# Performance work log

Hardware: AMD Instinct MI355X
Metric: run time of the kernel (lower is better)

## Reference

```python
import jax, jax.numpy as jnp
import numpy as np

# AccumulateKnn with distances == 1.0 everywhere and n_moments=0:
# weight w = exp(-distance) = exp(-1); output = concat(mean_k(w*f), max_k(w*f))
_W = float(np.exp(-1.0))


def _accumulate_knn(features, idx):
    # features: [N, F], idx: [N, K] -> [N, 2F]
    g = features[idx]                      # [N, K, F] neighbour gather
    mean = jnp.mean(g, axis=1) * _W        # [N, F]
    mx = jnp.max(g, axis=1) * _W           # [N, F]
    return jnp.concatenate([mean, mx], axis=-1)


def setup_inputs() -> dict:
    key = jax.random.key(0)
    k1, k2, k3, k4 = jax.random.split(key, 4)
    N, K, F = 200000, 32, 64
    x = jax.random.normal(k1, (N, F), dtype=jnp.float32)
    neighbour_indices = jax.random.randint(k2, (N, K), 0, N, dtype=jnp.int64)
    W0 = jax.random.normal(k3, (F, 64), dtype=jnp.float32) * (1.0 / np.sqrt(F))
    b0 = jnp.zeros((64,), dtype=jnp.float32)
    W1 = jax.random.normal(k4, (128, 64), dtype=jnp.float32) * (1.0 / np.sqrt(128))
    b1 = jnp.zeros((64,), dtype=jnp.float32)
    return {"x": x, "neighbour_indices": neighbour_indices,
            "W0": W0, "b0": b0, "W1": W1, "b1": b1}


def reference(x, neighbour_indices, W0, b0, W1, b1):
    allfeat = []
    feats = x
    for (W, b) in ((W0, b0), (W1, b1)):
        f = jax.nn.relu(feats @ W + b)            # dense + ReLU, [N, F_i]
        coll = _accumulate_knn(f, neighbour_indices)  # [N, 2*F_i]
        # subtract tiled self features: tile(f,[1,2]) == concat([f,f],-1)
        out = coll - jnp.concatenate([f, f], axis=-1)
        allfeat.append(out)
        feats = out
    return jnp.concatenate(allfeat + [x], axis=-1)  # [N, 128+128+64]
```

## Files before the change

kernel.cpp:

```cpp
#include <hip/hip_runtime.h>
#include <hip/hip_bf16.h>

typedef __hip_bfloat16 bf16;
typedef __attribute__((ext_vector_type(8))) short short8;
typedef __attribute__((ext_vector_type(4))) float f32x4;

__device__ __forceinline__ float us2f(unsigned short u) {
  union { unsigned int ui; float f; } cv; cv.ui = ((unsigned int)u) << 16; return cv.f;
}
__device__ __forceinline__ unsigned short f2us(float f) {
  union { float f; unsigned int u; } cv; cv.f = f;
  unsigned int u = cv.u;
  return (unsigned short)((u + 0x7fffu + ((u >> 16) & 1u)) >> 16);
}
__device__ __forceinline__ float lo2f(unsigned int u) {
  union { unsigned int ui; float f; } cv; cv.ui = u << 16; return cv.f;
}
__device__ __forceinline__ float hi2f(unsigned int u) {
  union { unsigned int ui; float f; } cv; cv.ui = u & 0xffff0000u; return cv.f;
}

#define WEXP 0.36787944117144233f

template<int KDIM>
__global__ __launch_bounds__(256) void dense_mfma_kernel(
    const float* __restrict__ in, int in_stride,
    const float* __restrict__ W, const float* __restrict__ b,
    bf16* __restrict__ fout, float* __restrict__ xcopy, int n)
{
  constexpr int NKS = KDIM / 32;
  constexpr int NFRAG = NKS * 4 * 64;
  __shared__ unsigned short WTf[NFRAG * 8];

  const int tx = threadIdx.x;
#pragma unroll
  for (int fch = 0; fch < NFRAG / 256; ++fch) {
    const int fi = fch * 256 + tx;
    const int ln = fi & 63;
    const int ct = (fi >> 6) & 3;
    const int ks = fi >> 8;
    const int c  = ct * 16 + (ln & 15);
    const int kb = ks * 32 + (ln >> 4) * 8;
    short8 wf;
#pragma unroll
    for (int j = 0; j < 8; ++j)
      wf[j] = (short)f2us(W[(size_t)(kb + j) * 64 + c]);
    *(short8*)&WTf[(size_t)fi * 8] = wf;
  }
  __syncthreads();

  const int wv = tx >> 6;
  const int lane = tx & 63;
  const int mrow = lane & 15;
  const int kgrp = lane >> 4;
  const int row = blockIdx.x * 64 + wv * 16 + mrow;

  f32x4 acc[4] = {};

#pragma unroll
  for (int ks = 0; ks < NKS; ++ks) {
    const int k0 = ks * 32 + kgrp * 8;
    float4 a0 = make_float4(0.f, 0.f, 0.f, 0.f);
    float4 a1 = make_float4(0.f, 0.f, 0.f, 0.f);
    if (row < n) {
      a0 = *(const float4*)(in + (size_t)row * in_stride + k0);
      a1 = *(const float4*)(in + (size_t)row * in_stride + k0 + 4);
    }
    if (xcopy != nullptr && row < n) {
      *(float4*)(xcopy + (size_t)row * 320 + k0) = a0;
      *(float4*)(xcopy + (size_t)row * 320 + k0 + 4) = a1;
    }
    short8 xhi, xlo;
    const float av[8] = {a0.x, a0.y, a0.z, a0.w, a1.x, a1.y, a1.z, a1.w};
#pragma unroll
    for (int j = 0; j < 8; ++j) {
      const unsigned short h = f2us(av[j]);
      xhi[j] = (short)h;
      xlo[j] = (short)f2us(av[j] - us2f(h));
    }
#pragma unroll
    for (int ct = 0; ct < 4; ++ct) {
      const short8 wfr = *(const short8*)&WTf[(size_t)((ks * 4 + ct) * 64 + lane) * 8];
      acc[ct] = __builtin_amdgcn_mfma_f32_16x16x32_bf16(wfr, xhi, acc[ct], 0, 0, 0);
      acc[ct] = __builtin_amdgcn_mfma_f32_16x16x32_bf16(wfr, xlo, acc[ct], 0, 0, 0);
    }
  }

  if (row < n) {
    unsigned short* fr = (unsigned short*)fout + (size_t)row * 64;
#pragma unroll
    for (int ct = 0; ct < 4; ++ct) {
      const int c0 = ct * 16 + kgrp * 4;
      const float4 bb = *(const float4*)&b[c0];
      ushort4 o;
      o.x = f2us(fmaxf(acc[ct][0] + bb.x, 0.f));
      o.y = f2us(fmaxf(acc[ct][1] + bb.y, 0.f));
      o.z = f2us(fmaxf(acc[ct][2] + bb.z, 0.f));
      o.w = f2us(fmaxf(acc[ct][3] + bb.w, 0.f));
      *(ushort4*)&fr[c0] = o;
    }
  }
}

__global__ __launch_bounds__(256) void accum_kernel(
    const bf16* __restrict__ f,
    const int* __restrict__ idx,
    float* __restrict__ out,
    int n)
{
  const int wid = threadIdx.x >> 6;
  const int lane = threadIdx.x & 63;
  const int i = blockIdx.x * 4 + wid;
  if (i >= n) return;

  int iv = 0;
  if (lane < 32) iv = idx[(size_t)i * 32 + lane];

  const int L = lane & 7;
  const int srcbase = (lane >> 3) << 2;
  const char* fb = (const char*)f;

  const uint4 sd = *(const uint4*)(fb + (((unsigned)i) << 7) + ((unsigned)L << 4));

  int nk[4];
#pragma unroll
  for (int t = 0; t < 4; ++t) nk[t] = __shfl(iv, srcbase + t);

  uint4 d[4];
#pragma unroll
  for (int t = 0; t < 4; ++t)
    d[t] = *(const uint4*)(fb + (((unsigned)nk[t]) << 7) + ((unsigned)L << 4));

  float s[8], m[8];
#pragma unroll
  for (int j = 0; j < 8; ++j) { s[j] = 0.f; m[j] = -3.4e38f; }
#pragma unroll
  for (int t = 0; t < 4; ++t) {
    float v;
    v = lo2f(d[t].x); s[0] += v; m[0] = fmaxf(m[0], v);
    v = hi2f(d[t].x); s[1] += v; m[1] = fmaxf(m[1], v);
    v = lo2f(d[t].y); s[2] += v; m[2] = fmaxf(m[2], v);
    v = hi2f(d[t].y); s[3] += v; m[3] = fmaxf(m[3], v);
    v = lo2f(d[t].z); s[4] += v; m[4] = fmaxf(m[4], v);
    v = hi2f(d[t].z); s[5] += v; m[5] = fmaxf(m[5], v);
    v = lo2f(d[t].w); s[6] += v; m[6] = fmaxf(m[6], v);
    v = hi2f(d[t].w); s[7] += v; m[7] = fmaxf(m[7], v);
  }

#pragma unroll
  for (int off = 8; off <= 32; off <<= 1) {
#pragma unroll
    for (int j = 0; j < 8; ++j) {
      s[j] += __shfl_xor(s[j], off);
      m[j] = fmaxf(m[j], __shfl_xor(m[j], off));
    }
  }

  float self[8];
  self[0] = lo2f(sd.x); self[1] = hi2f(sd.x);
  self[2] = lo2f(sd.y); self[3] = hi2f(sd.y);
  self[4] = lo2f(sd.z); self[5] = hi2f(sd.z);
  self[6] = lo2f(sd.w); self[7] = hi2f(sd.w);

  const float cmean = WEXP / 32.0f;
  const int o = lane >> 3;
  float* orow = out + (size_t)i * 320;
  if (o == 0) {
    float4 a, bq;
    a.x = s[0] * cmean - self[0]; a.y = s[1] * cmean - self[1];
    a.z = s[2] * cmean - self[2]; a.w = s[3] * cmean - self[3];
    bq.x = s[4] * cmean - self[4]; bq.y = s[5] * cmean - self[5];
    bq.z = s[6] * cmean - self[6]; bq.w = s[7] * cmean - self[7];
    *(float4*)(orow + 8 * L) = a;
    *(float4*)(orow + 8 * L + 4) = bq;
  } else if (o == 1) {
    float4 a, bq;
    a.x = m[0] * WEXP - self[0]; a.y = m[1] * WEXP - self[1];
    a.z = m[2] * WEXP - self[2]; a.w = m[3] * WEXP - self[3];
    bq.x = m[4] * WEXP - self[4]; bq.y = m[5] * WEXP - self[5];
    bq.z = m[6] * WEXP - self[6]; bq.w = m[7] * WEXP - self[7];
    *(float4*)(orow + 64 + 8 * L) = a;
    *(float4*)(orow + 64 + 8 * L + 4) = bq;
  }
}

extern "C" void kernel_launch(void* const* d_in, const int* in_sizes, int n_in,
                              void* d_out, int out_size, void* d_ws, size_t ws_size,
                              hipStream_t stream) {
  const float* x  = (const float*)d_in[0];
  const int* idx  = (const int*)d_in[1];
  const float* W0 = (const float*)d_in[2];
  const float* b0 = (const float*)d_in[3];
  const float* W1 = (const float*)d_in[4];
  const float* b1 = (const float*)d_in[5];
  float* out = (float*)d_out;
  const int n = in_sizes[0] / 64;

  bf16* fbuf = (bf16*)d_ws;

  const int dblocks = (n + 63) / 64;
  const int ablocks = (n + 3) / 4;

  dense_mfma_kernel<64><<<dblocks, 256, 0, stream>>>(x, 64, W0, b0, fbuf, out + 256, n);
  accum_kernel<<<ablocks, 256, 0, stream>>>(fbuf, idx, out, n);
  dense_mfma_kernel<128><<<dblocks, 256, 0, stream>>>(out, 320, W1, b1, fbuf, nullptr, n);
  accum_kernel<<<ablocks, 256, 0, stream>>>(fbuf, idx, out + 128, n);
}
```

Before: 558.5 us.

## Fuse first kNN accumulation with second dense layer via shared memory

Merges the first accumulate kernel and the second dense MFMA kernel into one kernel. Each 64-row block gathers neighbours, writes the layer-1 output to global memory and also to shared memory, then runs the dense matmul from LDS, so the 128-wide activations are not re-read from global. Gathers are software-pipelined across two register sets, and a second workspace buffer holds the layer-2 features. The fused kernel uses much more shared memory per block (about 50 KB), which may lower occupancy for the latency-bound gather.

```diff
diff --git a/kernel.cpp b/kernel.cpp
--- a/kernel.cpp
+++ b/kernel.cpp
@@ -88,6 +88,204 @@
 
   if (row < n) {
     unsigned short* fr = (unsigned short*)fout + (size_t)row * 64;
+#pragma unroll
+    for (int ct = 0; ct < 4; ++ct) {
+      const int c0 = ct * 16 + kgrp * 4;
+      const float4 bb = *(const float4*)&b[c0];
+      ushort4 o;
+      o.x = f2us(fmaxf(acc[ct][0] + bb.x, 0.f));
+      o.y = f2us(fmaxf(acc[ct][1] + bb.y, 0.f));
+      o.z = f2us(fmaxf(acc[ct][2] + bb.z, 0.f));
+      o.w = f2us(fmaxf(acc[ct][3] + bb.w, 0.f));
+      *(ushort4*)&fr[c0] = o;
+    }
+  }
+}
+
+__global__ __launch_bounds__(256) void accum_dense_fused_kernel(
+    const bf16* __restrict__ f0,
+    const int* __restrict__ idx,
+    const float* __restrict__ W,
+    const float* __restrict__ b,
+    float* __restrict__ out,
+    bf16* __restrict__ f1,
+    int n)
+{
+  __shared__ unsigned short WTf[1024 * 8];
+  __shared__ float SX[64][132];
+
+  const int tx = threadIdx.x;
+  const int p0 = blockIdx.x * 64;
+
+#pragma unroll
+  for (int fch = 0; fch < 4; ++fch) {
+    const int fi = fch * 256 + tx;
+    const int ln = fi & 63;
+    const int ct = (fi >> 6) & 3;
+    const int ks = fi >> 8;
+    const int c  = ct * 16 + (ln & 15);
+    const int kb = ks * 32 + (ln >> 4) * 8;
+    short8 wf;
+#pragma unroll
+    for (int j = 0; j < 8; ++j)
+      wf[j] = (short)f2us(W[(size_t)(kb + j) * 64 + c]);
+    *(short8*)&WTf[(size_t)fi * 8] = wf;
+  }
+
+  const int wv = tx >> 6;
+  const int lane = tx & 63;
+  const int oct = lane >> 3;
+  const unsigned Lo16 = ((unsigned)(lane & 7)) << 4;
+  const char* fb = (const char*)f0;
+  const float cmean = WEXP / 32.0f;
+
+  const uint4* idxv = (const uint4*)(idx + (size_t)(p0 + wv * 16) * 32);
+  uint4 q0 = make_uint4(0u, 0u, 0u, 0u), q1 = make_uint4(0u, 0u, 0u, 0u);
+  if (p0 + wv * 16 + (lane >> 3) < n)     q0 = idxv[lane];
+  if (p0 + wv * 16 + 8 + (lane >> 3) < n) q1 = idxv[64 + lane];
+
+#define ISSUE(pt, SD, D0, D1, D2, D3)                                        \
+  {                                                                          \
+    const uint4 q = ((pt) < 8) ? q0 : q1;                                    \
+    const int srcl = (((pt) & 7) << 3) + oct;                                \
+    const int n0 = __shfl((int)q.x, srcl);                                   \
+    const int n1 = __shfl((int)q.y, srcl);                                   \
+    const int n2 = __shfl((int)q.z, srcl);                                   \
+    const int n3 = __shfl((int)q.w, srcl);                                   \
+    const int ii = p0 + wv * 16 + (pt);                                      \
+    if (ii < n) {                                                            \
+      SD = *(const uint4*)(fb + (((unsigned)ii) << 7) + Lo16);               \
+      D0 = *(const uint4*)(fb + (((unsigned)n0) << 7) + Lo16);               \
+      D1 = *(const uint4*)(fb + (((unsigned)n1) << 7) + Lo16);               \
+      D2 = *(const uint4*)(fb + (((unsigned)n2) << 7) + Lo16);               \
+      D3 = *(const uint4*)(fb + (((unsigned)n3) << 7) + Lo16);               \
+    }                                                                        \
+  }
+
+#define UNP(D)                                                               \
+  { float v;                                                                 \
+    v = lo2f(D.x); s0 += v; m0 = fmaxf(m0, v);                               \
+    v = hi2f(D.x); s1 += v; m1 = fmaxf(m1, v);                               \
+    v = lo2f(D.y); s2 += v; m2 = fmaxf(m2, v);                               \
+    v = hi2f(D.y); s3 += v; m3 = fmaxf(m3, v);                               \
+    v = lo2f(D.z); s4 += v; m4 = fmaxf(m4, v);                               \
+    v = hi2f(D.z); s5 += v; m5 = fmaxf(m5, v);                               \
+    v = lo2f(D.w); s6 += v; m6 = fmaxf(m6, v);                               \
+    v = hi2f(D.w); s7 += v; m7 = fmaxf(m7, v); }
+
+#define BFLY(off)                                                            \
+  { s0 += __shfl_xor(s0, off); m0 = fmaxf(m0, __shfl_xor(m0, off));          \
+    s1 += __shfl_xor(s1, off); m1 = fmaxf(m1, __shfl_xor(m1, off));          \
+    s2 += __shfl_xor(s2, off); m2 = fmaxf(m2, __shfl_xor(m2, off));          \
+    s3 += __shfl_xor(s3, off); m3 = fmaxf(m3, __shfl_xor(m3, off));          \
+    s4 += __shfl_xor(s4, off); m4 = fmaxf(m4, __shfl_xor(m4, off));          \
+    s5 += __shfl_xor(s5, off); m5 = fmaxf(m5, __shfl_xor(m5, off));          \
+    s6 += __shfl_xor(s6, off); m6 = fmaxf(m6, __shfl_xor(m6, off));          \
+    s7 += __shfl_xor(s7, off); m7 = fmaxf(m7, __shfl_xor(m7, off)); }
+
+#define REDUCE(pt, SD, D0, D1, D2, D3)                                       \
+  {                                                                          \
+    float s0 = 0.f, s1 = 0.f, s2 = 0.f, s3 = 0.f,                            \
+          s4 = 0.f, s5 = 0.f, s6 = 0.f, s7 = 0.f;                            \
+    float m0 = -3.4e38f, m1 = -3.4e38f, m2 = -3.4e38f, m3 = -3.4e38f,        \
+          m4 = -3.4e38f, m5 = -3.4e38f, m6 = -3.4e38f, m7 = -3.4e38f;        \
+    UNP(D0) UNP(D1) UNP(D2) UNP(D3)                                          \
+    BFLY(8) BFLY(16) BFLY(32)                                                \
+    const int ii = p0 + wv * 16 + (pt);                                      \
+    if (ii < n) {                                                            \
+      float4 a, bq;                                                          \
+      if (oct == 0) {                                                        \
+        a.x  = s0 * cmean - lo2f(SD.x); a.y  = s1 * cmean - hi2f(SD.x);      \
+        a.z  = s2 * cmean - lo2f(SD.y); a.w  = s3 * cmean - hi2f(SD.y);      \
+        bq.x = s4 * cmean - lo2f(SD.z); bq.y = s5 * cmean - hi2f(SD.z);      \
+        bq.z = s6 * cmean - lo2f(SD.w); bq.w = s7 * cmean - hi2f(SD.w);      \
+        float* orow = out + (size_t)ii * 320 + 8 * (lane & 7);               \
+        *(float4*)orow = a; *(float4*)(orow + 4) = bq;                       \
+        float* sx = &SX[wv * 16 + (pt)][8 * (lane & 7)];                     \
+        *(float4*)sx = a; *(float4*)(sx + 4) = bq;                           \
+      } else if (oct == 1) {                                                 \
+        a.x  = m0 * WEXP - lo2f(SD.x); a.y  = m1 * WEXP - hi2f(SD.x);        \
+        a.z  = m2 * WEXP - lo2f(SD.y); a.w  = m3 * WEXP - hi2f(SD.y);        \
+        bq.x = m4 * WEXP - lo2f(SD.z); bq.y = m5 * WEXP - hi2f(SD.z);        \
+        bq.z = m6 * WEXP - lo2f(SD.w); bq.w = m7 * WEXP - hi2f(SD.w);        \
+        float* orow = out + (size_t)ii * 320 + 64 + 8 * (lane & 7);          \
+        *(float4*)orow = a; *(float4*)(orow + 4) = bq;                       \
+        float* sx = &SX[wv * 16 + (pt)][64 + 8 * (lane & 7)];                \
+        *(float4*)sx = a; *(float4*)(sx + 4) = bq;                           \
+      }                                                                      \
+    }                                                                        \
+  }
+
+  {
+    uint4 sA, a0, a1, a2, a3, sB, b0q, b1q, b2q, b3q;
+    ISSUE(0, sA, a0, a1, a2, a3)
+    ISSUE(1, sB, b0q, b1q, b2q, b3q)
+    REDUCE(0, sA, a0, a1, a2, a3)
+    ISSUE(2, sA, a0, a1, a2, a3)
+    REDUCE(1, sB, b0q, b1q, b2q, b3q)
+    ISSUE(3, sB, b0q, b1q, b2q, b3q)
+    REDUCE(2, sA, a0, a1, a2, a3)
+    ISSUE(4, sA, a0, a1, a2, a3)
+    REDUCE(3, sB, b0q, b1q, b2q, b3q)
+    ISSUE(5, sB, b0q, b1q, b2q, b3q)
+    REDUCE(4, sA, a0, a1, a2, a3)
+    ISSUE(6, sA, a0, a1, a2, a3)
+    REDUCE(5, sB, b0q, b1q, b2q, b3q)
+    ISSUE(7, sB, b0q, b1q, b2q, b3q)
+    REDUCE(6, sA, a0, a1, a2, a3)
+    ISSUE(8, sA, a0, a1, a2, a3)
+    REDUCE(7, sB, b0q, b1q, b2q, b3q)
+    ISSUE(9, sB, b0q, b1q, b2q, b3q)
+    REDUCE(8, sA, a0, a1, a2, a3)
+    ISSUE(10, sA, a0, a1, a2, a3)
+    REDUCE(9, sB, b0q, b1q, b2q, b3q)
+    ISSUE(11, sB, b0q, b1q, b2q, b3q)
+    REDUCE(10, sA, a0, a1, a2, a3)
+    ISSUE(12, sA, a0, a1, a2, a3)
+    REDUCE(11, sB, b0q, b1q, b2q, b3q)
+    ISSUE(13, sB, b0q, b1q, b2q, b3q)
+    REDUCE(12, sA, a0, a1, a2, a3)
+    ISSUE(14, sA, a0, a1, a2, a3)
+    REDUCE(13, sB, b0q, b1q, b2q, b3q)
+    ISSUE(15, sB, b0q, b1q, b2q, b3q)
+    REDUCE(14, sA, a0, a1, a2, a3)
+    REDUCE(15, sB, b0q, b1q, b2q, b3q)
+  }
+#undef ISSUE
+#undef UNP
+#undef BFLY
+#undef REDUCE
+
+  __syncthreads();
+
+  const int mrow = lane & 15;
+  const int kgrp = lane >> 4;
+  const int row = p0 + wv * 16 + mrow;
+
+  f32x4 acc[4] = {};
+#pragma unroll
+  for (int ks = 0; ks < 4; ++ks) {
+    const int k0 = ks * 32 + kgrp * 8;
+    const float4 a0 = *(const float4*)&SX[wv * 16 + mrow][k0];
+    const float4 a1 = *(const float4*)&SX[wv * 16 + mrow][k0 + 4];
+    short8 xhi, xlo;
+    const float av[8] = {a0.x, a0.y, a0.z, a0.w, a1.x, a1.y, a1.z, a1.w};
+#pragma unroll
+    for (int j = 0; j < 8; ++j) {
+      const unsigned short h = f2us(av[j]);
+      xhi[j] = (short)h;
+      xlo[j] = (short)f2us(av[j] - us2f(h));
+    }
+#pragma unroll
+    for (int ct = 0; ct < 4; ++ct) {
+      const short8 wfr = *(const short8*)&WTf[(size_t)((ks * 4 + ct) * 64 + lane) * 8];
+      acc[ct] = __builtin_amdgcn_mfma_f32_16x16x32_bf16(wfr, xhi, acc[ct], 0, 0, 0);
+      acc[ct] = __builtin_amdgcn_mfma_f32_16x16x32_bf16(wfr, xlo, acc[ct], 0, 0, 0);
+    }
+  }
+
+  if (row < n) {
+    unsigned short* fr = (unsigned short*)f1 + (size_t)row * 64;
 #pragma unroll
     for (int ct = 0; ct < 4; ++ct) {
       const int c0 = ct * 16 + kgrp * 4;
@@ -196,13 +394,13 @@
   float* out = (float*)d_out;
   const int n = in_sizes[0] / 64;
 
-  bf16* fbuf = (bf16*)d_ws;
+  bf16* fbuf0 = (bf16*)d_ws;
+  bf16* fbuf1 = (bf16*)((char*)d_ws + (size_t)n * 64 * 2);
 
   const int dblocks = (n + 63) / 64;
   const int ablocks = (n + 3) / 4;
 
-  dense_mfma_kernel<64><<<dblocks, 256, 0, stream>>>(x, 64, W0, b0, fbuf, out + 256, n);
-  accum_kernel<<<ablocks, 256, 0, stream>>>(fbuf, idx, out, n);
-  dense_mfma_kernel<128><<<dblocks, 256, 0, stream>>>(out, 320, W1, b1, fbuf, nullptr, n);
-  accum_kernel<<<ablocks, 256, 0, stream>>>(fbuf, idx, out + 128, n);
-}
+  dense_mfma_kernel<64><<<dblocks, 256, 0, stream>>>(x, 64, W0, b0, fbuf0, out + 256, n);
+  accum_dense_fused_kernel<<<dblocks, 256, 0, stream>>>(fbuf0, idx, W1, b1, out, fbuf1, n);
+  accum_kernel<<<ablocks, 256, 0, stream>>>(fbuf1, idx, out + 128, n);
+}
```

After: 570.1 us. 1.02x slower.
